# Kernel optimization log

Measured on AMD Instinct MI355X. Metric: run time of the kernel, lower is better.

The kernel has to match this reference:

```python
import jax, jax.numpy as jnp
import numpy as np

N = 50000      # nodes
E = 800000     # edges (before self loops)
IN = 128       # in_ch
HID = 128      # hid (conv1 concat output)
OUT = 128      # out_ch
H = 4          # heads in conv1
NEG_SLOPE = 0.2


def setup_inputs() -> dict:
    key = jax.random.key(0)
    ks = jax.random.split(key, 16)
    s = 0.05
    return {
        "x": jax.random.normal(ks[0], (N, IN), dtype=jnp.float32),
        "edge_index": jax.random.randint(ks[1], (2, E), 0, N, dtype=jnp.int64),
        # conv1 params (heads=4, per-head dim HID//H)
        "W1l": jax.random.normal(ks[2], (IN, HID), dtype=jnp.float32) * s,
        "b1l": jnp.zeros((HID,), jnp.float32),
        "W1r": jax.random.normal(ks[3], (IN, HID), dtype=jnp.float32) * s,
        "b1r": jnp.zeros((HID,), jnp.float32),
        "att1": jax.random.normal(ks[4], (H, HID // H), dtype=jnp.float32) * s,
        "bias1": jnp.zeros((HID,), jnp.float32),
        # conv2 params (heads=1)
        "W2l": jax.random.normal(ks[5], (HID, OUT), dtype=jnp.float32) * s,
        "b2l": jnp.zeros((OUT,), jnp.float32),
        "W2r": jax.random.normal(ks[6], (HID, OUT), dtype=jnp.float32) * s,
        "b2r": jnp.zeros((OUT,), jnp.float32),
        "att2": jax.random.normal(ks[7], (1, OUT), dtype=jnp.float32) * s,
        "bias2": jnp.zeros((OUT,), jnp.float32),
    }


def gatv2_conv(x, src, dst, Wl, bl, Wr, br, att, heads):
    """PyG GATv2Conv (share_weights=False, concat=True).
    message(j->i): e = LeakyReLU(x_l[j] + x_r[i]); logit = <e, att>;
    softmax over edges per destination i; out_i = sum alpha * x_l[j].
    """
    n = x.shape[0]
    c = Wl.shape[1] // heads
    xl = (x @ Wl + bl).reshape(n, heads, c)   # source transform
    xr = (x @ Wr + br).reshape(n, heads, c)   # destination transform
    e = jax.nn.leaky_relu(xl[src] + xr[dst], NEG_SLOPE)      # [E, H, C]
    logits = jnp.einsum("ehc,hc->eh", e, att)                 # [E, H]
    m = jax.lax.stop_gradient(
        jax.ops.segment_max(logits, dst, num_segments=n))     # [N, H]
    p = jnp.exp(logits - m[dst])                              # [E, H]
    denom = jax.ops.segment_sum(p, dst, num_segments=n)       # [N, H]
    alpha = p / denom[dst]                                    # [E, H]
    out = jax.ops.segment_sum(xl[src] * alpha[..., None], dst,
                              num_segments=n)                 # [N, H, C]
    return out.reshape(n, heads * c)


def reference(x, edge_index, W1l, b1l, W1r, b1r, att1, bias1,
              W2l, b2l, W2r, b2r, att2, bias2):
    n = x.shape[0]
    # PyG default add_self_loops=True
    loops = jnp.arange(n, dtype=edge_index.dtype)
    src = jnp.concatenate([edge_index[0], loops])
    dst = jnp.concatenate([edge_index[1], loops])
    h = gatv2_conv(x, src, dst, W1l, b1l, W1r, b1r, att1, H) + bias1
    h = jax.nn.relu(h)
    out = gatv2_conv(h, src, dst, W2l, b2l, W2r, b2r, att2, 1) + bias2
    return out
```

## Files before the change

kernel.cpp:

```cpp
#include <hip/hip_runtime.h>
#include <hip/hip_bf16.h>

#define NODES 50000
#define NEDGE 800000
#define CH 128
#define NEG_SLOPE 0.2f
#define SCAN_CHUNK 2048
#define NBLK ((NODES + SCAN_CHUNK - 1) / SCAN_CHUNK)
#define NINF -1.0e30f
#define LOG2E 1.44269504088896340736f
#define RESCALE_THR 8.0f
#define NSLICE 400
#define SSLICE (NEDGE / NSLICE)
#define HSLICE 4000
#define NHS (NEDGE / HSLICE)
#define ZB ((NODES + 255) / 256)
#define GR 64
#define GGC ((NODES + GR - 1) / GR)
#define GB 391
#define HROWS (GB * GR)
#define LDP 136

typedef short short8 __attribute__((ext_vector_type(8)));
typedef float f32x4 __attribute__((ext_vector_type(4)));
typedef float f32x2 __attribute__((ext_vector_type(2)));

__device__ __forceinline__ unsigned fbits(float f) {
    union { float f; unsigned u; } v; v.f = f; return v.u;
}
__device__ __forceinline__ float asf(unsigned u) {
    union { float f; unsigned u; } v; v.u = u; return v.f;
}
__device__ __forceinline__ unsigned short f2bf(float f) {
    unsigned u = fbits(f);
    unsigned r = u + 0x7fff + ((u >> 16) & 1);
    return (unsigned short)(r >> 16);
}
__device__ __forceinline__ float bf2f(unsigned short h) {
    return asf(((unsigned)h) << 16);
}
__device__ __forceinline__ void bf8cvt2(uint4 u, f32x2* f) {
    f[0] = (f32x2){asf(u.x << 16), asf(u.x & 0xFFFF0000u)};
    f[1] = (f32x2){asf(u.y << 16), asf(u.y & 0xFFFF0000u)};
    f[2] = (f32x2){asf(u.z << 16), asf(u.z & 0xFFFF0000u)};
    f[3] = (f32x2){asf(u.w << 16), asf(u.w & 0xFFFF0000u)};
}
__device__ __forceinline__ int dset(int dst) {
    return (int)(((unsigned)dst * 8u) / 50000u);
}

__global__ __launch_bounds__(256) void prep_kernel(const void* idx, int* flag,
                                                   int* cnt,
                                                   const float* __restrict__ W0,
                                                   const float* __restrict__ W1,
                                                   const float* __restrict__ W2,
                                                   const float* __restrict__ W3,
                                                   unsigned short* __restrict__ wbase) {
    int b = (int)blockIdx.x;
    if (b < ZB) {
        int t = b * 256 + (int)threadIdx.x;
        if (t < NODES) cnt[t] = 0;
        if (b == 0 && threadIdx.x < 64) {
            const int* w = (const int*)idx;
            int nz = (w[2 * threadIdx.x + 1] != 0) ? 1 : 0;
            unsigned long long bal = __ballot(nz);
            if (threadIdx.x == 0) *flag = (bal == 0ull) ? 1 : 0;
        }
        return;
    }
    int wb = b - ZB;
    int which = wb >> 6;
    const float* W = (which == 0) ? W0 : (which == 1) ? W1 : (which == 2) ? W2 : W3;
    unsigned short* hiT = wbase + (size_t)which * 32768;
    unsigned short* loT = hiT + 16384;
    int i = (wb & 63) * 256 + (int)threadIdx.x;
    int k = i >> 7, n = i & 127;
    float f = W[i];
    unsigned short h = f2bf(f);
    unsigned short l = f2bf(f - bf2f(h));
    hiT[n * CH + k] = h;
    loT[n * CH + k] = l;
}

__global__ __launch_bounds__(256) void scan1_kernel(const int* __restrict__ cnt,
                                                    int* __restrict__ bsum) {
    int base = blockIdx.x * SCAN_CHUNK + (int)threadIdx.x * 8;
    int s = 0;
    #pragma unroll
    for (int k = 0; k < 8; ++k) {
        int i = base + k;
        s += (i < NODES) ? cnt[i] : 0;
    }
    #pragma unroll
    for (int m = 1; m < 64; m <<= 1) s += __shfl_xor(s, m);
    __shared__ int ws[4];
    if ((threadIdx.x & 63) == 0) ws[threadIdx.x >> 6] = s;
    __syncthreads();
    if (threadIdx.x == 0) bsum[blockIdx.x] = ws[0] + ws[1] + ws[2] + ws[3];
}

__global__ __launch_bounds__(256) void scan3_kernel(const int* __restrict__ cnt,
                                                    const int* __restrict__ bsum,
                                                    int* __restrict__ offs,
                                                    int* __restrict__ cursor) {
    int tid = (int)threadIdx.x;
    int bpre = 0;
    #pragma unroll
    for (int b = 0; b < NBLK; ++b) bpre += (b < (int)blockIdx.x) ? bsum[b] : 0;

    int base = blockIdx.x * SCAN_CHUNK + tid * 8;
    int v[8];
    int s = 0;
    #pragma unroll
    for (int k = 0; k < 8; ++k) {
        int i = base + k;
        v[k] = (i < NODES) ? cnt[i] : 0;
        s += v[k];
    }
    int lane = tid & 63;
    int incl = s;
    #pragma unroll
    for (int m = 1; m < 64; m <<= 1) {
        int t = __shfl_up(incl, m);
        if (lane >= m) incl += t;
    }
    __shared__ int wtot[4];
    if (lane == 63) wtot[tid >> 6] = incl;
    __syncthreads();
    int w = tid >> 6;
    int wbase = 0;
    #pragma unroll
    for (int k = 0; k < 4; ++k) wbase += (k < w) ? wtot[k] : 0;
    int excl = bpre + wbase + (incl - s);
    #pragma unroll
    for (int k = 0; k < 8; ++k) {
        int i = base + k;
        if (i < NODES) { offs[i] = excl; cursor[i] = excl; }
        excl += v[k];
    }
    if (blockIdx.x == 0 && tid == 0) offs[NODES] = NEDGE;
}

__device__ __forceinline__ void gemm1_role(
        int r0, int tid,
        unsigned short (*xh)[LDP], unsigned short (*xlo)[LDP],
        const float* __restrict__ X,
        const unsigned short* __restrict__ whTl, const unsigned short* __restrict__ wlTl,
        const unsigned short* __restrict__ whTr, const unsigned short* __restrict__ wlTr,
        const float* __restrict__ bl, const float* __restrict__ br,
        unsigned short* __restrict__ Ylb, float* __restrict__ Yr, int nrows) {
    {
        int row = tid >> 3;
        int c0 = (tid & 7) * 16;
        const float* src = X + (size_t)(r0 + row) * CH + c0;
        bool valid = (r0 + row) < nrows;
        #pragma unroll
        for (int j = 0; j < 16; j += 4) {
            float4 v = valid ? *(const float4*)(src + j)
                             : make_float4(0.f, 0.f, 0.f, 0.f);
            unsigned ux = fbits(v.x), uy = fbits(v.y);
            unsigned uz = fbits(v.z), uw = fbits(v.w);
            unsigned hx = ux & 0xFFFF0000u, hy = uy & 0xFFFF0000u;
            unsigned hz = uz & 0xFFFF0000u, hw = uw & 0xFFFF0000u;
            uint2 hp;
            hp.x = (ux >> 16) | hy;
            hp.y = (uz >> 16) | hw;
            float lx = v.x - asf(hx), ly = v.y - asf(hy);
            float lz = v.z - asf(hz), lw = v.w - asf(hw);
            uint2 lp;
            lp.x = (fbits(lx) >> 16) | (fbits(ly) & 0xFFFF0000u);
            lp.y = (fbits(lz) >> 16) | (fbits(lw) & 0xFFFF0000u);
            *(uint2*)&xh[row][c0 + j]  = hp;
            *(uint2*)&xlo[row][c0 + j] = lp;
        }
    }
    __syncthreads();

    int wave = tid >> 6;
    int lane = tid & 63;
    int l15 = lane & 15, q = lane >> 4;

    f32x4 acc[4][2];
    #pragma unroll
    for (int mt = 0; mt < 4; ++mt)
        #pragma unroll
        for (int nt = 0; nt < 2; ++nt) acc[mt][nt] = (f32x4)0.f;

    const unsigned short* bhp[2];
    const unsigned short* blp_[2];
    int ncol[2];
    #pragma unroll
    for (int nt = 0; nt < 2; ++nt) {
        int n = (wave * 2 + nt) * 16 + l15;
        ncol[nt] = n;
        int nn = n & 127;
        bhp[nt]  = ((n < CH) ? whTl : whTr) + (size_t)nn * CH;
        blp_[nt] = ((n < CH) ? wlTl : wlTr) + (size_t)nn * CH;
    }

    for (int kt = 0; kt < 4; ++kt) {
        int kofs = kt * 32 + q * 8;
        short8 ah[4], al[4];
        #pragma unroll
        for (int mt = 0; mt < 4; ++mt) {
            ah[mt] = *(const short8*)&xh[mt * 16 + l15][kofs];
            al[mt] = *(const short8*)&xlo[mt * 16 + l15][kofs];
        }
        #pragma unroll
        for (int nt = 0; nt < 2; ++nt) {
            short8 bh8 = *(const short8*)(bhp[nt] + kofs);
            short8 bl8 = *(const short8*)(blp_[nt] + kofs);
            #pragma unroll
            for (int mt = 0; mt < 4; ++mt) {
                acc[mt][nt] = __builtin_amdgcn_mfma_f32_16x16x32_bf16(
                                  ah[mt], bh8, acc[mt][nt], 0, 0, 0);
                acc[mt][nt] = __builtin_amdgcn_mfma_f32_16x16x32_bf16(
                                  al[mt], bh8, acc[mt][nt], 0, 0, 0);
                acc[mt][nt] = __builtin_amdgcn_mfma_f32_16x16x32_bf16(
                                  ah[mt], bl8, acc[mt][nt], 0, 0, 0);
            }
        }
    }

    #pragma unroll
    for (int nt = 0; nt < 2; ++nt) {
        int n = ncol[nt];
        int nc = n & 127;
        if (n < CH) {
            float bv = bl[nc];
            #pragma unroll
            for (int mt = 0; mt < 4; ++mt)
                #pragma unroll
                for (int reg = 0; reg < 4; ++reg) {
                    int row = r0 + mt * 16 + q * 4 + reg;
                    if (row < nrows)
                        Ylb[(size_t)row * CH + nc] = f2bf(acc[mt][nt][reg] + bv);
                }
        } else {
            float bv = br[nc];
            #pragma unroll
            for (int mt = 0; mt < 4; ++mt)
                #pragma unroll
                for (int reg = 0; reg < 4; ++reg) {
                    int row = r0 + mt * 16 + q * 4 + reg;
                    if (row < nrows)
                        Yr[(size_t)row * CH + nc] = acc[mt][nt][reg] + bv;
                }
        }
    }
}

__global__ __launch_bounds__(512) void gemm1a_hist(
        const float* __restrict__ X,
        const unsigned short* __restrict__ whTl, const unsigned short* __restrict__ wlTl,
        const unsigned short* __restrict__ whTr, const unsigned short* __restrict__ wlTr,
        const float* __restrict__ bl, const float* __restrict__ br,
        unsigned short* __restrict__ Ylb, float* __restrict__ Yr, int nrows,
        const void* idx, const int* flag, int* cnt) {
    __shared__ unsigned short xh[GR][LDP];
    __shared__ unsigned short xlo[GR][LDP];

    if (blockIdx.x >= GB) {
        int set = (int)blockIdx.x & 7;
        int slice = ((int)blockIdx.x - GB) >> 3;
        int base = slice * HSLICE;
        int endE = base + HSLICE;
        int i64 = *flag;
        const int* w = (const int*)idx;
        for (int e = base + (int)threadIdx.x; e < endE; e += 512) {
            int dst = i64 ? w[2 * (NEDGE + e)] : w[NEDGE + e];
            if (dset(dst) == set) atomicAdd(&cnt[dst], 1);
        }
        return;
    }
    gemm1_role(blockIdx.x * GR, (int)threadIdx.x, xh, xlo,
               X, whTl, wlTl, whTr, wlTr, bl, br, Ylb, Yr, nrows);
}

__global__ __launch_bounds__(512) void gemm1b_scatter(
        const float* __restrict__ X,
        const unsigned short* __restrict__ whTl, const unsigned short* __restrict__ wlTl,
        const unsigned short* __restrict__ whTr, const unsigned short* __restrict__ wlTr,
        const float* __restrict__ bl, const float* __restrict__ br,
        unsigned short* __restrict__ Ylb, float* __restrict__ Yr, int nrows,
        const void* idx, const int* flag, int* cursor, int* __restrict__ srcs) {
    __shared__ unsigned short xh[GR][LDP];
    __shared__ unsigned short xlo[GR][LDP];

    if (blockIdx.x >= GB) {
        int set = (int)blockIdx.x & 7;
        int slice = ((int)blockIdx.x - GB) >> 3;
        int base = slice * SSLICE;
        int endE = base + SSLICE;
        int i64 = *flag;
        const int* w = (const int*)idx;
        for (int e = base + (int)threadIdx.x; e < endE; e += 512) {
            int dst = i64 ? w[2 * (NEDGE + e)] : w[NEDGE + e];
            if (dset(dst) == set) {
                int src = i64 ? w[2 * e] : w[e];
                int pos = atomicAdd(&cursor[dst], 1);
                srcs[pos] = src;
            }
        }
        return;
    }
    gemm1_role(HROWS + blockIdx.x * GR, (int)threadIdx.x, xh, xlo,
               X, whTl, wlTl, whTr, wlTr, bl, br, Ylb, Yr, nrows);
}

__global__ __launch_bounds__(512) void gemm_dual_mfma_pl(
        const unsigned short* __restrict__ Ah, const unsigned short* __restrict__ Al,
        const unsigned short* __restrict__ whTl, const unsigned short* __restrict__ wlTl,
        const unsigned short* __restrict__ whTr, const unsigned short* __restrict__ wlTr,
        const float* __restrict__ bl, const float* __restrict__ br,
        unsigned short* __restrict__ Ylb, float* __restrict__ Yr, int nrows) {
    __shared__ unsigned short xh[GR][LDP];
    __shared__ unsigned short xlo[GR][LDP];

    int r0 = blockIdx.x * GR;
    int tid = (int)threadIdx.x;

    {
        int row = tid >> 3;
        int c0 = (tid & 7) * 16;
        int gr = r0 + row;
        if (gr > nrows - 1) gr = nrows - 1;
        const uint4* ph = (const uint4*)(Ah + (size_t)gr * CH + c0);
        const uint4* pl = (const uint4*)(Al + (size_t)gr * CH + c0);
        uint4 h0 = ph[0], h1 = ph[1];
        uint4 l0 = pl[0], l1 = pl[1];
        *(uint4*)&xh[row][c0]      = h0;
        *(uint4*)&xh[row][c0 + 8]  = h1;
        *(uint4*)&xlo[row][c0]     = l0;
        *(uint4*)&xlo[row][c0 + 8] = l1;
    }
    __syncthreads();

    int wave = tid >> 6;
    int lane = tid & 63;
    int l15 = lane & 15, q = lane >> 4;

    f32x4 acc[4][2];
    #pragma unroll
    for (int mt = 0; mt < 4; ++mt)
        #pragma unroll
        for (int nt = 0; nt < 2; ++nt) acc[mt][nt] = (f32x4)0.f;

    const unsigned short* bhp[2];
    const unsigned short* blp_[2];
    int ncol[2];
    #pragma unroll
    for (int nt = 0; nt < 2; ++nt) {
        int n = (wave * 2 + nt) * 16 + l15;
        ncol[nt] = n;
        int nn = n & 127;
        bhp[nt]  = ((n < CH) ? whTl : whTr) + (size_t)nn * CH;
        blp_[nt] = ((n < CH) ? wlTl : wlTr) + (size_t)nn * CH;
    }

    for (int kt = 0; kt < 4; ++kt) {
        int kofs = kt * 32 + q * 8;
        short8 ah[4], al[4];
        #pragma unroll
        for (int mt = 0; mt < 4; ++mt) {
            ah[mt] = *(const short8*)&xh[mt * 16 + l15][kofs];
            al[mt] = *(const short8*)&xlo[mt * 16 + l15][kofs];
        }
        #pragma unroll
        for (int nt = 0; nt < 2; ++nt) {
            short8 bh8 = *(const short8*)(bhp[nt] + kofs);
            short8 bl8 = *(const short8*)(blp_[nt] + kofs);
            #pragma unroll
            for (int mt = 0; mt < 4; ++mt) {
                acc[mt][nt] = __builtin_amdgcn_mfma_f32_16x16x32_bf16(
                                  ah[mt], bh8, acc[mt][nt], 0, 0, 0);
                acc[mt][nt] = __builtin_amdgcn_mfma_f32_16x16x32_bf16(
                                  al[mt], bh8, acc[mt][nt], 0, 0, 0);
                acc[mt][nt] = __builtin_amdgcn_mfma_f32_16x16x32_bf16(
                                  ah[mt], bl8, acc[mt][nt], 0, 0, 0);
            }
        }
    }

    #pragma unroll
    for (int nt = 0; nt < 2; ++nt) {
        int n = ncol[nt];
        int nc = n & 127;
        if (n < CH) {
            float bv = bl[nc];
            #pragma unroll
            for (int mt = 0; mt < 4; ++mt)
                #pragma unroll
                for (int reg = 0; reg < 4; ++reg) {
                    int row = r0 + mt * 16 + q * 4 + reg;
                    if (row < nrows)
                        Ylb[(size_t)row * CH + nc] = f2bf(acc[mt][nt][reg] + bv);
                }
        } else {
            float bv = br[nc];
            #pragma unroll
            for (int mt = 0; mt < 4; ++mt)
                #pragma unroll
                for (int reg = 0; reg < 4; ++reg) {
                    int row = r0 + mt * 16 + q * 4 + reg;
                    if (row < nrows)
                        Yr[(size_t)row * CH + nc] = acc[mt][nt][reg] + bv;
                }
        }
    }
}

template <int HEADS, bool RELU, bool SPLITOUT>
__global__ __launch_bounds__(256) void node_pass(
        const unsigned short* __restrict__ xlb,
        const float* __restrict__ xr,
        const float* __restrict__ att,
        const float* __restrict__ bias,
        const int* __restrict__ offs, const int* __restrict__ srcs,
        float* __restrict__ outf,
        unsigned short* __restrict__ outh, unsigned short* __restrict__ outl) {
    constexpr int GL = (CH / HEADS) / 8;
    int wave = (int)threadIdx.x >> 6;
    int i = blockIdx.x * 4 + wave;
    int lane = (int)threadIdx.x & 63;
    int g = lane >> 4;
    int l16 = lane & 15;
    int c0 = l16 * 8;

    f32x2 r2[4], a2[4], s2[4];
    {
        const float4* xrp = (const float4*)(xr + (size_t)i * CH + c0);
        float4 r0 = xrp[0], r1 = xrp[1];
        r2[0] = (f32x2){r0.x, r0.y}; r2[1] = (f32x2){r0.z, r0.w};
        r2[2] = (f32x2){r1.x, r1.y}; r2[3] = (f32x2){r1.z, r1.w};
        const float4* atp = (const float4*)(att + c0);
        float4 a0 = atp[0], a1 = atp[1];
        a2[0] = (f32x2){a0.x, a0.y} * LOG2E; a2[1] = (f32x2){a0.z, a0.w} * LOG2E;
        a2[2] = (f32x2){a1.x, a1.y} * LOG2E; a2[3] = (f32x2){a1.z, a1.w} * LOG2E;
    }
    uint4 us = *(const uint4*)(xlb + (size_t)i * CH + c0);
    bf8cvt2(us, s2);

    f32x2 td = (f32x2)0.f;
    #pragma unroll
    for (int k = 0; k < 4; ++k) {
        f32x2 z = s2[k] + r2[k];
        f32x2 l = __builtin_elementwise_max(z, z * NEG_SLOPE);
        td += l * a2[k];
    }
    float ts = td.x + td.y;
    #pragma unroll
    for (int msk = 1; msk < GL; msk <<= 1) ts += __shfl_xor(ts, msk);

    float m = ts;
    float d = (g == 0) ? 1.f : 0.f;
    f32x2 acc2[4];
    #pragma unroll
    for (int k = 0; k < 4; ++k) acc2[k] = (g == 0) ? s2[k] : (f32x2)0.f;

    int beg = offs[i], end = offs[i + 1];
    int deg = end - beg;
    int iters = (deg + 3) >> 2;
    if (iters > 0) {
        int last = end - 1;
        int e = beg + g;
        int si = srcs[min(e, last)];
        uint4 u = *(const uint4*)(xlb + (size_t)si * CH + c0);

        for (int it = 0; it < iters; ++it, e += 4) {
            bool valid = e < end;
            int sn = srcs[min(e + 4, last)];
            uint4 un = *(const uint4*)(xlb + (size_t)sn * CH + c0);

            f32x2 f2[4];
            bf8cvt2(u, f2);
            f32x2 td2 = (f32x2)0.f;
            #pragma unroll
            for (int k = 0; k < 4; ++k) {
                f32x2 z = f2[k] + r2[k];
                f32x2 l = __builtin_elementwise_max(z, z * NEG_SLOPE);
                td2 += l * a2[k];
            }
            float t = td2.x + td2.y;
            #pragma unroll
            for (int msk = 1; msk < GL; msk <<= 1) t += __shfl_xor(t, msk);
            t = valid ? t : NINF;

            if (__any(t > m + RESCALE_THR)) {
                float nm = fmaxf(m, t);
                float sc = exp2f(m - nm);
                float p  = exp2f(t - nm);
                d = d * sc + p;
                #pragma unroll
                for (int k = 0; k < 4; ++k) acc2[k] = acc2[k] * sc + f2[k] * p;
                m = nm;
            } else {
                float p = exp2f(t - m);
                d += p;
                #pragma unroll
                for (int k = 0; k < 4; ++k) acc2[k] += f2[k] * p;
            }
            u = un;
        }
    }

    #pragma unroll
    for (int msk = 16; msk <= 32; msk <<= 1) {
        float mo  = __shfl_xor(m, msk);
        float dof = __shfl_xor(d, msk);
        float nm = fmaxf(m, mo);
        float s0 = exp2f(m - nm), s1 = exp2f(mo - nm);
        d = d * s0 + dof * s1;
        #pragma unroll
        for (int k = 0; k < 4; ++k) {
            f32x2 ao;
            ao.x = __shfl_xor(acc2[k].x, msk);
            ao.y = __shfl_xor(acc2[k].y, msk);
            acc2[k] = acc2[k] * s0 + ao * s1;
        }
        m = nm;
    }

    if (g == 0) {
        float inv = 1.0f / d;
        const float4* bp = (const float4*)(bias + c0);
        float4 b0 = bp[0], b1 = bp[1];
        float bb[8] = {b0.x, b0.y, b0.z, b0.w, b1.x, b1.y, b1.z, b1.w};
        float o[8];
        #pragma unroll
        for (int k = 0; k < 4; ++k) {
            o[2*k]   = acc2[k].x * inv + bb[2*k];
            o[2*k+1] = acc2[k].y * inv + bb[2*k+1];
        }
        #pragma unroll
        for (int c = 0; c < 8; ++c)
            if (RELU) o[c] = fmaxf(o[c], 0.f);
        if (SPLITOUT) {
            unsigned hu[8];
            float lo[8];
            #pragma unroll
            for (int c = 0; c < 8; ++c) {
                hu[c] = fbits(o[c]) & 0xFFFF0000u;
                lo[c] = o[c] - asf(hu[c]);
            }
            uint4 ph, pl;
            ph.x = (hu[0] >> 16) | hu[1];  ph.y = (hu[2] >> 16) | hu[3];
            ph.z = (hu[4] >> 16) | hu[5];  ph.w = (hu[6] >> 16) | hu[7];
            pl.x = (fbits(lo[0]) >> 16) | (fbits(lo[1]) & 0xFFFF0000u);
            pl.y = (fbits(lo[2]) >> 16) | (fbits(lo[3]) & 0xFFFF0000u);
            pl.z = (fbits(lo[4]) >> 16) | (fbits(lo[5]) & 0xFFFF0000u);
            pl.w = (fbits(lo[6]) >> 16) | (fbits(lo[7]) & 0xFFFF0000u);
            *(uint4*)(outh + (size_t)i * CH + c0) = ph;
            *(uint4*)(outl + (size_t)i * CH + c0) = pl;
        } else {
            float4 w0 = make_float4(o[0], o[1], o[2], o[3]);
            float4 w1 = make_float4(o[4], o[5], o[6], o[7]);
            float4* op = (float4*)(outf + (size_t)i * CH + c0);
            op[0] = w0; op[1] = w1;
        }
    }
}

extern "C" void kernel_launch(void* const* d_in, const int* in_sizes, int n_in,
                              void* d_out, int out_size, void* d_ws, size_t ws_size,
                              hipStream_t stream) {
    const float* x     = (const float*)d_in[0];
    const void*  eidx  = d_in[1];
    const float* W1l   = (const float*)d_in[2];
    const float* b1l   = (const float*)d_in[3];
    const float* W1r   = (const float*)d_in[4];
    const float* b1r   = (const float*)d_in[5];
    const float* att1  = (const float*)d_in[6];
    const float* bias1 = (const float*)d_in[7];
    const float* W2l   = (const float*)d_in[8];
    const float* b2l   = (const float*)d_in[9];
    const float* W2r   = (const float*)d_in[10];
    const float* b2r   = (const float*)d_in[11];
    const float* att2  = (const float*)d_in[12];
    const float* bias2 = (const float*)d_in[13];
    float* out = (float*)d_out;

    unsigned short* xlb = (unsigned short*)d_ws;
    float* xr = (float*)(xlb + (size_t)NODES * CH);
    unsigned short* hbh = (unsigned short*)(xr + (size_t)NODES * CH);
    unsigned short* hbl = hbh + (size_t)NODES * CH;
    int* offs   = (int*)(hbl + (size_t)NODES * CH);
    int* cnt    = offs + (NODES + 1);
    int* cursor = cnt + NODES;
    int* srcs   = cursor + NODES;
    int* flag   = srcs + NEDGE;
    int* bsum   = flag + 1;
    unsigned short* wbuf =
        (unsigned short*)(((uintptr_t)(bsum + NBLK) + 15) & ~(uintptr_t)15);
    unsigned short* w1lh = wbuf;              unsigned short* w1ll = wbuf + 16384;
    unsigned short* w1rh = wbuf + 32768;      unsigned short* w1rl = wbuf + 49152;
    unsigned short* w2lh = wbuf + 65536;      unsigned short* w2ll = wbuf + 81920;
    unsigned short* w2rh = wbuf + 98304;      unsigned short* w2rl = wbuf + 114688;

    const int FGA = GB + NHS * 8;
    const int FGB = GB + NSLICE * 8;

    prep_kernel<<<ZB + 256, 256, 0, stream>>>(eidx, flag, cnt,
                                              W1l, W1r, W2l, W2r, wbuf);

    gemm1a_hist<<<FGA, 512, 0, stream>>>(x, w1lh, w1ll, w1rh, w1rl,
                                         b1l, b1r, xlb, xr, NODES,
                                         eidx, flag, cnt);

    scan1_kernel<<<NBLK, 256, 0, stream>>>(cnt, bsum);
    scan3_kernel<<<NBLK, 256, 0, stream>>>(cnt, bsum, offs, cursor);

    gemm1b_scatter<<<FGB, 512, 0, stream>>>(x, w1lh, w1ll, w1rh, w1rl,
                                            b1l, b1r, xlb, xr, NODES,
                                            eidx, flag, cursor, srcs);

    node_pass<4, true, true><<<(NODES + 3) / 4, 256, 0, stream>>>(
        xlb, xr, att1, bias1, offs, srcs, nullptr, hbh, hbl);

    gemm_dual_mfma_pl<<<GGC, 512, 0, stream>>>(hbh, hbl, w2lh, w2ll, w2rh, w2rl,
                                               b2l, b2r, xlb, xr, NODES);
    node_pass<1, false, false><<<(NODES + 3) / 4, 256, 0, stream>>>(
        xlb, xr, att2, bias2, offs, srcs, out, nullptr, nullptr);
}
```

Before: 322.1 us.

## Overlap layer-2 GEMM with second half of layer-1 node pass

Splits the layer-1 node aggregation into two halves. The first half runs alone; the second half runs in one fused launch whose other blocks compute the layer-2 dual GEMM for the rows that are already finished. The remaining GEMM rows then run in a separate launch. To make this safe, the layer-2 source features go to a new workspace buffer, so the layer-1 source features that concurrent node blocks still gather stay intact. The goal is to fill idle compute units during the gather-bound pass and cut a serial gap. It costs extra workspace and one more launch, and it falls back to the old schedule when the workspace is too small.

```diff
diff --git a/kernel.cpp b/kernel.cpp
--- a/kernel.cpp
+++ b/kernel.cpp
@@ -19,6 +19,7 @@
 #define GGC ((NODES + GR - 1) / GR)
 #define GB 391
 #define HROWS (GB * GR)
+#define NPB ((NODES - HROWS) / 8)
 #define LDP 136
 
 typedef short short8 __attribute__((ext_vector_type(8)));
@@ -250,76 +251,14 @@
     }
 }
 
-__global__ __launch_bounds__(512) void gemm1a_hist(
-        const float* __restrict__ X,
+__device__ __forceinline__ void gemm_pl_role(
+        int r0, int tid,
+        unsigned short (*xh)[LDP], unsigned short (*xlo)[LDP],
+        const unsigned short* Ah, const unsigned short* Al,
         const unsigned short* __restrict__ whTl, const unsigned short* __restrict__ wlTl,
         const unsigned short* __restrict__ whTr, const unsigned short* __restrict__ wlTr,
         const float* __restrict__ bl, const float* __restrict__ br,
-        unsigned short* __restrict__ Ylb, float* __restrict__ Yr, int nrows,
-        const void* idx, const int* flag, int* cnt) {
-    __shared__ unsigned short xh[GR][LDP];
-    __shared__ unsigned short xlo[GR][LDP];
-
-    if (blockIdx.x >= GB) {
-        int set = (int)blockIdx.x & 7;
-        int slice = ((int)blockIdx.x - GB) >> 3;
-        int base = slice * HSLICE;
-        int endE = base + HSLICE;
-        int i64 = *flag;
-        const int* w = (const int*)idx;
-        for (int e = base + (int)threadIdx.x; e < endE; e += 512) {
-            int dst = i64 ? w[2 * (NEDGE + e)] : w[NEDGE + e];
-            if (dset(dst) == set) atomicAdd(&cnt[dst], 1);
-        }
-        return;
-    }
-    gemm1_role(blockIdx.x * GR, (int)threadIdx.x, xh, xlo,
-               X, whTl, wlTl, whTr, wlTr, bl, br, Ylb, Yr, nrows);
-}
-
-__global__ __launch_bounds__(512) void gemm1b_scatter(
-        const float* __restrict__ X,
-        const unsigned short* __restrict__ whTl, const unsigned short* __restrict__ wlTl,
-        const unsigned short* __restrict__ whTr, const unsigned short* __restrict__ wlTr,
-        const float* __restrict__ bl, const float* __restrict__ br,
-        unsigned short* __restrict__ Ylb, float* __restrict__ Yr, int nrows,
-        const void* idx, const int* flag, int* cursor, int* __restrict__ srcs) {
-    __shared__ unsigned short xh[GR][LDP];
-    __shared__ unsigned short xlo[GR][LDP];
-
-    if (blockIdx.x >= GB) {
-        int set = (int)blockIdx.x & 7;
-        int slice = ((int)blockIdx.x - GB) >> 3;
-        int base = slice * SSLICE;
-        int endE = base + SSLICE;
-        int i64 = *flag;
-        const int* w = (const int*)idx;
-        for (int e = base + (int)threadIdx.x; e < endE; e += 512) {
-            int dst = i64 ? w[2 * (NEDGE + e)] : w[NEDGE + e];
-            if (dset(dst) == set) {
-                int src = i64 ? w[2 * e] : w[e];
-                int pos = atomicAdd(&cursor[dst], 1);
-                srcs[pos] = src;
-            }
-        }
-        return;
-    }
-    gemm1_role(HROWS + blockIdx.x * GR, (int)threadIdx.x, xh, xlo,
-               X, whTl, wlTl, whTr, wlTr, bl, br, Ylb, Yr, nrows);
-}
-
-__global__ __launch_bounds__(512) void gemm_dual_mfma_pl(
-        const unsigned short* __restrict__ Ah, const unsigned short* __restrict__ Al,
-        const unsigned short* __restrict__ whTl, const unsigned short* __restrict__ wlTl,
-        const unsigned short* __restrict__ whTr, const unsigned short* __restrict__ wlTr,
-        const float* __restrict__ bl, const float* __restrict__ br,
-        unsigned short* __restrict__ Ylb, float* __restrict__ Yr, int nrows) {
-    __shared__ unsigned short xh[GR][LDP];
-    __shared__ unsigned short xlo[GR][LDP];
-
-    int r0 = blockIdx.x * GR;
-    int tid = (int)threadIdx.x;
-
+        unsigned short* Ylb, float* Yr, int nrows) {
     {
         int row = tid >> 3;
         int c0 = (tid & 7) * 16;
@@ -411,18 +350,13 @@
 }
 
 template <int HEADS, bool RELU, bool SPLITOUT>
-__global__ __launch_bounds__(256) void node_pass(
-        const unsigned short* __restrict__ xlb,
-        const float* __restrict__ xr,
-        const float* __restrict__ att,
-        const float* __restrict__ bias,
+__device__ __forceinline__ void node_body(
+        int i, int lane,
+        const unsigned short* xlb, const float* xr,
+        const float* __restrict__ att, const float* __restrict__ bias,
         const int* __restrict__ offs, const int* __restrict__ srcs,
-        float* __restrict__ outf,
-        unsigned short* __restrict__ outh, unsigned short* __restrict__ outl) {
+        float* outf, unsigned short* outh, unsigned short* outl) {
     constexpr int GL = (CH / HEADS) / 8;
-    int wave = (int)threadIdx.x >> 6;
-    int i = blockIdx.x * 4 + wave;
-    int lane = (int)threadIdx.x & 63;
     int g = lane >> 4;
     int l16 = lane & 15;
     int c0 = l16 * 8;
@@ -561,6 +495,114 @@
     }
 }
 
+__global__ __launch_bounds__(512) void gemm1a_hist(
+        const float* __restrict__ X,
+        const unsigned short* __restrict__ whTl, const unsigned short* __restrict__ wlTl,
+        const unsigned short* __restrict__ whTr, const unsigned short* __restrict__ wlTr,
+        const float* __restrict__ bl, const float* __restrict__ br,
+        unsigned short* __restrict__ Ylb, float* __restrict__ Yr, int nrows,
+        const void* idx, const int* flag, int* cnt) {
+    __shared__ unsigned short xh[GR][LDP];
+    __shared__ unsigned short xlo[GR][LDP];
+
+    if (blockIdx.x >= GB) {
+        int set = (int)blockIdx.x & 7;
+        int slice = ((int)blockIdx.x - GB) >> 3;
+        int base = slice * HSLICE;
+        int endE = base + HSLICE;
+        int i64 = *flag;
+        const int* w = (const int*)idx;
+        for (int e = base + (int)threadIdx.x; e < endE; e += 512) {
+            int dst = i64 ? w[2 * (NEDGE + e)] : w[NEDGE + e];
+            if (dset(dst) == set) atomicAdd(&cnt[dst], 1);
+        }
+        return;
+    }
+    gemm1_role(blockIdx.x * GR, (int)threadIdx.x, xh, xlo,
+               X, whTl, wlTl, whTr, wlTr, bl, br, Ylb, Yr, nrows);
+}
+
+__global__ __launch_bounds__(512) void gemm1b_scatter(
+        const float* __restrict__ X,
+        const unsigned short* __restrict__ whTl, const unsigned short* __restrict__ wlTl,
+        const unsigned short* __restrict__ whTr, const unsigned short* __restrict__ wlTr,
+        const float* __restrict__ bl, const float* __restrict__ br,
+        unsigned short* __restrict__ Ylb, float* __restrict__ Yr, int nrows,
+        const void* idx, const int* flag, int* cursor, int* __restrict__ srcs) {
+    __shared__ unsigned short xh[GR][LDP];
+    __shared__ unsigned short xlo[GR][LDP];
+
+    if (blockIdx.x >= GB) {
+        int set = (int)blockIdx.x & 7;
+        int slice = ((int)blockIdx.x - GB) >> 3;
+        int base = slice * SSLICE;
+        int endE = base + SSLICE;
+        int i64 = *flag;
+        const int* w = (const int*)idx;
+        for (int e = base + (int)threadIdx.x; e < endE; e += 512) {
+            int dst = i64 ? w[2 * (NEDGE + e)] : w[NEDGE + e];
+            if (dset(dst) == set) {
+                int src = i64 ? w[2 * e] : w[e];
+                int pos = atomicAdd(&cursor[dst], 1);
+                srcs[pos] = src;
+            }
+        }
+        return;
+    }
+    gemm1_role(HROWS + blockIdx.x * GR, (int)threadIdx.x, xh, xlo,
+               X, whTl, wlTl, whTr, wlTr, bl, br, Ylb, Yr, nrows);
+}
+
+__global__ __launch_bounds__(512) void gemm_pl_kernel(
+        const unsigned short* Ah, const unsigned short* Al,
+        const unsigned short* __restrict__ whTl, const unsigned short* __restrict__ wlTl,
+        const unsigned short* __restrict__ whTr, const unsigned short* __restrict__ wlTr,
+        const float* __restrict__ bl, const float* __restrict__ br,
+        unsigned short* Ylb, float* Yr, int nrows, int r0base) {
+    __shared__ unsigned short xh[GR][LDP];
+    __shared__ unsigned short xlo[GR][LDP];
+    gemm_pl_role(r0base + (int)blockIdx.x * GR, (int)threadIdx.x, xh, xlo,
+                 Ah, Al, whTl, wlTl, whTr, wlTr, bl, br, Ylb, Yr, nrows);
+}
+
+template <int HEADS, bool RELU, bool SPLITOUT>
+__global__ __launch_bounds__(256) void node_pass(
+        const unsigned short* xlb, const float* xr,
+        const float* __restrict__ att, const float* __restrict__ bias,
+        const int* __restrict__ offs, const int* __restrict__ srcs,
+        float* outf, unsigned short* outh, unsigned short* outl) {
+    int wave = (int)threadIdx.x >> 6;
+    int i = blockIdx.x * 4 + wave;
+    int lane = (int)threadIdx.x & 63;
+    node_body<HEADS, RELU, SPLITOUT>(i, lane, xlb, xr, att, bias, offs, srcs,
+                                     outf, outh, outl);
+}
+
+__global__ __launch_bounds__(512) void np1b_gplA(
+        const unsigned short* hbh, const unsigned short* hbl,
+        const unsigned short* __restrict__ w2lh, const unsigned short* __restrict__ w2ll,
+        const unsigned short* __restrict__ w2rh, const unsigned short* __restrict__ w2rl,
+        const float* __restrict__ b2l, const float* __restrict__ b2r,
+        unsigned short* xlb2, float* xr,
+        const unsigned short* xlb1,
+        const float* __restrict__ att1, const float* __restrict__ bias1,
+        const int* __restrict__ offs, const int* __restrict__ srcs) {
+    __shared__ unsigned short xh[GR][LDP];
+    __shared__ unsigned short xlo[GR][LDP];
+
+    if (blockIdx.x < GB) {
+        gemm_pl_role((int)blockIdx.x * GR, (int)threadIdx.x, xh, xlo,
+                     hbh, hbl, w2lh, w2ll, w2rh, w2rl, b2l, b2r,
+                     xlb2, xr, NODES);
+        return;
+    }
+    int wave = (int)threadIdx.x >> 6;
+    int i = HROWS + ((int)blockIdx.x - GB) * 8 + wave;
+    int lane = (int)threadIdx.x & 63;
+    node_body<4, true, true>(i, lane, xlb1, xr, att1, bias1, offs, srcs,
+                             nullptr, (unsigned short*)hbh, (unsigned short*)hbl);
+}
+
 extern "C" void kernel_launch(void* const* d_in, const int* in_sizes, int n_in,
                               void* d_out, int out_size, void* d_ws, size_t ws_size,
                               hipStream_t stream) {
@@ -596,6 +638,9 @@
     unsigned short* w1rh = wbuf + 32768;      unsigned short* w1rl = wbuf + 49152;
     unsigned short* w2lh = wbuf + 65536;      unsigned short* w2ll = wbuf + 81920;
     unsigned short* w2rh = wbuf + 98304;      unsigned short* w2rl = wbuf + 114688;
+    unsigned short* xlb2 = wbuf + 131072;
+    size_t need = (size_t)((char*)(xlb2 + (size_t)NODES * CH) - (char*)d_ws);
+    bool overlap = (ws_size >= need);
 
     const int FGA = GB + NHS * 8;
     const int FGB = GB + NSLICE * 8;
@@ -614,11 +659,22 @@
                                             b1l, b1r, xlb, xr, NODES,
                                             eidx, flag, cursor, srcs);
 
-    node_pass<4, true, true><<<(NODES + 3) / 4, 256, 0, stream>>>(
-        xlb, xr, att1, bias1, offs, srcs, nullptr, hbh, hbl);
-
-    gemm_dual_mfma_pl<<<GGC, 512, 0, stream>>>(hbh, hbl, w2lh, w2ll, w2rh, w2rl,
-                                               b2l, b2r, xlb, xr, NODES);
-    node_pass<1, false, false><<<(NODES + 3) / 4, 256, 0, stream>>>(
-        xlb, xr, att2, bias2, offs, srcs, out, nullptr, nullptr);
-}
+    if (overlap) {
+        node_pass<4, true, true><<<HROWS / 4, 256, 0, stream>>>(
+            xlb, xr, att1, bias1, offs, srcs, nullptr, hbh, hbl);
+        np1b_gplA<<<GB + NPB, 512, 0, stream>>>(
+            hbh, hbl, w2lh, w2ll, w2rh, w2rl, b2l, b2r, xlb2, xr,
+            xlb, att1, bias1, offs, srcs);
+        gemm_pl_kernel<<<GB, 512, 0, stream>>>(hbh, hbl, w2lh, w2ll, w2rh, w2rl,
+                                               b2l, b2r, xlb2, xr, NODES, HROWS);
+        node_pass<1, false, false><<<(NODES + 3) / 4, 256, 0, stream>>>(
+            xlb2, xr, att2, bias2, offs, srcs, out, nullptr, nullptr);
+    } else {
+        node_pass<4, true, true><<<(NODES + 3) / 4, 256, 0, stream>>>(
+            xlb, xr, att1, bias1, offs, srcs, nullptr, hbh, hbl);
+        gemm_pl_kernel<<<GGC, 512, 0, stream>>>(hbh, hbl, w2lh, w2ll, w2rh, w2rl,
+                                                b2l, b2r, xlb, xr, NODES, 0);
+        node_pass<1, false, false><<<(NODES + 3) / 4, 256, 0, stream>>>(
+            xlb, xr, att2, bias2, offs, srcs, out, nullptr, nullptr);
+    }
+}
```

Result: slower. 334.6 us (+3.9%).
